# Performance work log

Measured on AMD Instinct MI355X. Metric: run time of the kernel, lower is better.

Reference implementation:

```python
import jax, jax.numpy as jnp
import numpy as np
from jax import lax

K_NN = 16      # neighbors used by compute_knn_distance
ANCHOR_K = 64  # config['anchor_k']


def _knn_dist_vec(pts):
    """compute_knn_distance for one object: mean offset vector to K_NN nearest neighbors.
    pts: (N, 3) -> (N, 3)"""
    sq = jnp.sum(pts * pts, axis=-1)                      # (N,)
    d2 = sq[:, None] + sq[None, :] - 2.0 * (pts @ pts.T)  # (N, N) squared dists
    n = pts.shape[0]
    d2 = d2 + jnp.eye(n, dtype=pts.dtype) * 1e10          # exclude self
    _, idx = lax.top_k(-d2, K_NN)                          # (N, K_NN) nearest indices
    neigh = pts[idx]                                       # (N, K_NN, 3)
    return jnp.mean(neigh - pts[:, None, :], axis=1)       # (N, 3)


def _fps(pts, k):
    """Farthest point sampling for one object. pts: (N, 3) -> (k,) int32 indices."""
    d0 = jnp.sum((pts - pts[0]) ** 2, axis=-1)             # dist to seed point 0

    def step(min_d, _):
        idx = jnp.argmax(min_d)
        d = jnp.sum((pts - pts[idx]) ** 2, axis=-1)
        return jnp.minimum(min_d, d), idx

    _, idxs = lax.scan(step, d0, None, length=k - 1)
    return jnp.concatenate([jnp.zeros((1,), dtype=idxs.dtype), idxs])


def setup_inputs() -> dict:
    key = jax.random.key(0)
    k1, k2, k3, k4 = jax.random.split(key, 4)
    B, N_obj, N_v = 4, 8, 2048
    positions = jax.random.normal(k1, (B, N_obj, N_v, 3), dtype=jnp.float32)
    velocities = jax.random.normal(k2, (B, N_obj, N_v, 3), dtype=jnp.float32)
    physics_params = jax.random.uniform(k3, (B, N_obj, 3), dtype=jnp.float32)
    # reference pose at t=0: nearby but distinct so rel_pos is nontrivial
    ref_positions = positions + 0.05 * jax.random.normal(k4, (B, N_obj, N_v, 3), dtype=jnp.float32)
    return {"positions": positions, "velocities": velocities,
            "physics_params": physics_params, "ref_positions": ref_positions}


def reference(positions, velocities, physics_params, ref_positions):
    B, N_obj, N_v, _ = positions.shape
    flat = positions.reshape(B * N_obj, N_v, 3)

    # pairwise KNN distance feature per point
    dist_vec = jax.vmap(_knn_dist_vec)(flat).reshape(B, N_obj, N_v, 3)

    # iterative FPS anchor sampling (vectorized over all B*N_obj objects)
    anchors = jax.vmap(lambda p: _fps(p, ANCHOR_K))(flat).reshape(B, N_obj, ANCHOR_K)

    rel_pos = positions - ref_positions

    # multi-field gather at anchor indices (torch.gather on dim=2)
    gather = lambda f: jnp.take_along_axis(f, anchors[..., None], axis=2)
    anchor_dist = gather(dist_vec)       # (B, N_obj, K, 3)
    anchor_vel = gather(velocities)      # (B, N_obj, K, 3)
    anchor_rel = gather(rel_pos)         # (B, N_obj, K, 3)

    phys = jnp.broadcast_to(physics_params[:, :, None, :], (B, N_obj, ANCHOR_K, 3))
    query = jnp.concatenate([anchor_dist, anchor_vel, anchor_rel, phys], axis=-1)  # (B, N_obj, K, 12)
    return query
```

## Files before the change

### kernel.cpp

```cpp
#include <hip/hip_runtime.h>
#include <stdint.h>

#define NPTS 2048
#define KNN  16
#define AK   64
#define TPB  256
#define FPT  (NPTS / TPB)
#define KPL  (NPTS / 64)

typedef unsigned long long u64;
typedef unsigned int u32;

__device__ __forceinline__ float sq3(float x, float y, float z) {
    return __fadd_rn(__fadd_rn(__fmul_rn(x, x), __fmul_rn(y, y)), __fmul_rn(z, z));
}

__global__ __launch_bounds__(TPB) void fps_kernel(const float* __restrict__ pos,
                                                  int* __restrict__ anchors) {
    const int obj = blockIdx.x;
    const int t = threadIdx.x;
    __shared__ float sp[NPTS * 3];
    __shared__ u64 skey[8];

    {
        const float4* g4 = (const float4*)(pos + (size_t)obj * NPTS * 3);
        float4* s4 = (float4*)sp;
        #pragma unroll
        for (int i = 0; i < 6; i++) s4[t + i * TPB] = g4[t + i * TPB];
    }
    __syncthreads();

    float px[FPT], py[FPT], pz[FPT], mind[FPT];
    {
        const float ax0 = sp[0], ay0 = sp[1], az0 = sp[2];
        #pragma unroll
        for (int i = 0; i < FPT; i++) {
            const int j = t + i * TPB;
            px[i] = sp[j * 3 + 0];
            py[i] = sp[j * 3 + 1];
            pz[i] = sp[j * 3 + 2];
            mind[i] = sq3(__fsub_rn(px[i], ax0), __fsub_rn(py[i], ay0),
                          __fsub_rn(pz[i], az0));
        }
    }
    if (t == 0) anchors[obj * AK + 0] = 0;

    for (int s = 1; s < AK; s++) {
        float bv = mind[0];
        u32 slot = 0;
        #pragma unroll
        for (int i = 1; i < FPT; i++)
            if (mind[i] > bv) { bv = mind[i]; slot = (u32)i; }
        const u32 j = (u32)t + slot * TPB;
        u64 key = ((u64)__float_as_uint(bv) << 32) | (u32)(~j);

        #pragma unroll
        for (int off = 32; off > 0; off >>= 1) {
            const u64 o = (u64)__shfl_xor((long long)key, off, 64);
            if (o > key) key = o;
        }

        u64* sk = &skey[(s & 1) * 4];
        if ((t & 63) == 0) sk[t >> 6] = key;
        __syncthreads();

        u64 k = sk[0];
        if (sk[1] > k) k = sk[1];
        if (sk[2] > k) k = sk[2];
        if (sk[3] > k) k = sk[3];
        const int idx = (int)(~(u32)k);
        if (t == 0) anchors[obj * AK + s] = idx;

        const float bx = sp[idx * 3 + 0];
        const float by = sp[idx * 3 + 1];
        const float bz = sp[idx * 3 + 2];
        #pragma unroll
        for (int i = 0; i < FPT; i++) {
            const float d2 = sq3(__fsub_rn(px[i], bx), __fsub_rn(py[i], by),
                                 __fsub_rn(pz[i], bz));
            mind[i] = fminf(mind[i], d2);
        }
    }
}

__global__ __launch_bounds__(TPB) void knn_gather_kernel(
    const float* __restrict__ pos, const float* __restrict__ vel,
    const float* __restrict__ phys, const float* __restrict__ refp,
    const int* __restrict__ anchors, float* __restrict__ out) {
    const int t = threadIdx.x;
    const int wid = t >> 6, lane = t & 63;
    const int g = blockIdx.x * 4 + wid;
    const int obj = g >> 6;

    __shared__ float sp[NPTS * 3];
    {
        const float4* g4 = (const float4*)(pos + (size_t)obj * NPTS * 3);
        float4* s4 = (float4*)sp;
        #pragma unroll
        for (int i = 0; i < 6; i++) s4[t + i * TPB] = g4[t + i * TPB];
    }
    const int a = anchors[g];
    __syncthreads();

    const float ax = sp[a * 3 + 0], ay = sp[a * 3 + 1], az = sp[a * 3 + 2];
    const float sqa = sq3(ax, ay, az);

    u32 b[KPL];
    #pragma unroll
    for (int i = 0; i < KPL; i++) {
        const int j = lane + i * 64;
        const float x = sp[j * 3 + 0], y = sp[j * 3 + 1], z = sp[j * 3 + 2];
        const float sqj = sq3(x, y, z);
        const float dot = __fadd_rn(
            __fadd_rn(__fmul_rn(ax, x), __fmul_rn(ay, y)), __fmul_rn(az, z));
        const float d2 = __fsub_rn(__fadd_rn(sqa, sqj), __fmul_rn(2.0f, dot));
        u32 bb = __float_as_uint(d2);
        bb ^= (bb & 0x80000000u) ? 0xFFFFFFFFu : 0x80000000u;
        b[i] = (j == a) ? 0xFFFFFFFFu : bb;
    }

    float sx = 0.0f, sy = 0.0f, sz = 0.0f;
    int winj = -1;

    for (int r = 0; r < KNN; r++) {
        const int wm = winj - lane;
        u32 bv = 0xFFFFFFFFu;
        u32 slot = 0;
        #pragma unroll
        for (int i = 0; i < KPL; i++) {
            if (wm == i * 64) b[i] = 0xFFFFFFFFu;
            if (b[i] < bv) { bv = b[i]; slot = (u32)i; }
        }
        u64 key = ((u64)bv << 32) | (u32)(lane + slot * 64);
        #pragma unroll
        for (int off = 32; off > 0; off >>= 1) {
            const u64 o = (u64)__shfl_xor((long long)key, off, 64);
            if (o < key) key = o;
        }
        winj = (int)(u32)key;

        const float wx = sp[winj * 3 + 0];
        const float wy = sp[winj * 3 + 1];
        const float wz = sp[winj * 3 + 2];
        sx = __fadd_rn(sx, __fsub_rn(wx, ax));
        sy = __fadd_rn(sy, __fsub_rn(wy, ay));
        sz = __fadd_rn(sz, __fsub_rn(wz, az));
    }

    if (lane == 0) {
        float* o = out + (size_t)g * 12;
        o[0] = __fmul_rn(sx, 0.0625f);
        o[1] = __fmul_rn(sy, 0.0625f);
        o[2] = __fmul_rn(sz, 0.0625f);
        const size_t base = (size_t)obj * NPTS * 3 + (size_t)a * 3;
        o[3] = vel[base + 0];
        o[4] = vel[base + 1];
        o[5] = vel[base + 2];
        o[6] = __fsub_rn(pos[base + 0], refp[base + 0]);
        o[7] = __fsub_rn(pos[base + 1], refp[base + 1]);
        o[8] = __fsub_rn(pos[base + 2], refp[base + 2]);
        const float* ph = phys + (size_t)obj * 3;
        o[9]  = ph[0];
        o[10] = ph[1];
        o[11] = ph[2];
    }
}

extern "C" void kernel_launch(void* const* d_in, const int* in_sizes, int n_in,
                              void* d_out, int out_size, void* d_ws, size_t ws_size,
                              hipStream_t stream) {
    const float* pos  = (const float*)d_in[0];
    const float* vel  = (const float*)d_in[1];
    const float* phys = (const float*)d_in[2];
    const float* refp = (const float*)d_in[3];
    float* out = (float*)d_out;

    const int n_obj = in_sizes[2] / 3;
    int* anchors = (int*)d_ws;

    fps_kernel<<<n_obj, TPB, 0, stream>>>(pos, anchors);
    knn_gather_kernel<<<n_obj * AK / 4, TPB, 0, stream>>>(pos, vel, phys, refp,
                                                          anchors, out);
}
```

Measured before the change: 115.5 us.

## Use DPP wave reductions, SoA shared layout, fused FPS argmax, per-lane top-4 KNN cache

FPS now folds the argmax into the distance-update loop. It also publishes each wave winner's coordinates alongside its key, so the post-barrier LDS lookup goes away. Both kernels store points in structure-of-arrays shared memory and use DPP-based wave reductions in place of some shuffles. In KNN, each lane keeps a sorted cache of its four smallest keys, so most rounds need only a wave min with no rescan of all 32 candidates; a lane rescans only when its cache runs dry. The catch is 64-bit keys that raise register pressure, and uncoalesced strided global loads into SoA.

Result: faster. 109.6 us (-5.2%).

```diff
diff --git a/kernel.cpp b/kernel.cpp
--- a/kernel.cpp
+++ b/kernel.cpp
@@ -10,76 +10,112 @@
 
 typedef unsigned long long u64;
 typedef unsigned int u32;
+#define UMAX 0xFFFFFFFFFFFFFFFFull
 
 __device__ __forceinline__ float sq3(float x, float y, float z) {
     return __fadd_rn(__fadd_rn(__fmul_rn(x, x), __fmul_rn(y, y)), __fmul_rn(z, z));
+}
+
+template <int CTRL>
+__device__ __forceinline__ u64 dpp64(u64 k) {
+    const int lo = __builtin_amdgcn_update_dpp((int)(u32)k, (int)(u32)k,
+                                               CTRL, 0xF, 0xF, false);
+    const int hi = __builtin_amdgcn_update_dpp((int)(u32)(k >> 32),
+                                               (int)(u32)(k >> 32),
+                                               CTRL, 0xF, 0xF, false);
+    return ((u64)(u32)hi << 32) | (u32)lo;
+}
+
+__device__ __forceinline__ u64 wave_max64(u64 k) {
+    u64 o;
+    o = dpp64<0xB1>(k);  if (o > k) k = o;
+    o = dpp64<0x4E>(k);  if (o > k) k = o;
+    o = dpp64<0x141>(k); if (o > k) k = o;
+    o = dpp64<0x140>(k); if (o > k) k = o;
+    o = (u64)__shfl_xor((long long)k, 16, 64); if (o > k) k = o;
+    o = (u64)__shfl_xor((long long)k, 32, 64); if (o > k) k = o;
+    return k;
+}
+
+__device__ __forceinline__ u64 wave_min64(u64 k) {
+    u64 o;
+    o = dpp64<0xB1>(k);  if (o < k) k = o;
+    o = dpp64<0x4E>(k);  if (o < k) k = o;
+    o = dpp64<0x141>(k); if (o < k) k = o;
+    o = dpp64<0x140>(k); if (o < k) k = o;
+    o = (u64)__shfl_xor((long long)k, 16, 64); if (o < k) k = o;
+    o = (u64)__shfl_xor((long long)k, 32, 64); if (o < k) k = o;
+    return k;
 }
 
 __global__ __launch_bounds__(TPB) void fps_kernel(const float* __restrict__ pos,
                                                   int* __restrict__ anchors) {
     const int obj = blockIdx.x;
     const int t = threadIdx.x;
-    __shared__ float sp[NPTS * 3];
+    const int wid = t >> 6, lane = t & 63;
+
+    __shared__ float sX[NPTS], sY[NPTS], sZ[NPTS];
     __shared__ u64 skey[8];
-
+    __shared__ float4 scrd[8];
+
+    const float* pts = pos + (size_t)obj * NPTS * 3;
+    #pragma unroll
+    for (int i = 0; i < FPT; i++) {
+        const int j = t + i * TPB;
+        sX[j] = pts[j * 3 + 0];
+        sY[j] = pts[j * 3 + 1];
+        sZ[j] = pts[j * 3 + 2];
+    }
+    __syncthreads();
+
+    float px[FPT], py[FPT], pz[FPT], mind[FPT];
+    u64 key;
     {
-        const float4* g4 = (const float4*)(pos + (size_t)obj * NPTS * 3);
-        float4* s4 = (float4*)sp;
-        #pragma unroll
-        for (int i = 0; i < 6; i++) s4[t + i * TPB] = g4[t + i * TPB];
-    }
-    __syncthreads();
-
-    float px[FPT], py[FPT], pz[FPT], mind[FPT];
-    {
-        const float ax0 = sp[0], ay0 = sp[1], az0 = sp[2];
+        const float ax0 = sX[0], ay0 = sY[0], az0 = sZ[0];
+        float bv = -1.0f; u32 bj = 0;
         #pragma unroll
         for (int i = 0; i < FPT; i++) {
             const int j = t + i * TPB;
-            px[i] = sp[j * 3 + 0];
-            py[i] = sp[j * 3 + 1];
-            pz[i] = sp[j * 3 + 2];
-            mind[i] = sq3(__fsub_rn(px[i], ax0), __fsub_rn(py[i], ay0),
-                          __fsub_rn(pz[i], az0));
-        }
+            px[i] = sX[j]; py[i] = sY[j]; pz[i] = sZ[j];
+            const float d2 = sq3(__fsub_rn(px[i], ax0), __fsub_rn(py[i], ay0),
+                                 __fsub_rn(pz[i], az0));
+            mind[i] = d2;
+            if (d2 > bv) { bv = d2; bj = (u32)j; }
+        }
+        key = ((u64)__float_as_uint(bv) << 32) | (u32)(~bj);
     }
     if (t == 0) anchors[obj * AK + 0] = 0;
 
     for (int s = 1; s < AK; s++) {
-        float bv = mind[0];
-        u32 slot = 0;
-        #pragma unroll
-        for (int i = 1; i < FPT; i++)
-            if (mind[i] > bv) { bv = mind[i]; slot = (u32)i; }
-        const u32 j = (u32)t + slot * TPB;
-        u64 key = ((u64)__float_as_uint(bv) << 32) | (u32)(~j);
-
-        #pragma unroll
-        for (int off = 32; off > 0; off >>= 1) {
-            const u64 o = (u64)__shfl_xor((long long)key, off, 64);
-            if (o > key) key = o;
-        }
-
-        u64* sk = &skey[(s & 1) * 4];
-        if ((t & 63) == 0) sk[t >> 6] = key;
+        const u64 wk = wave_max64(key);
+        const int side = (s & 1) * 4;
+        if (lane == 0) {
+            const int widx = (int)(~(u32)wk);
+            skey[side + wid] = wk;
+            scrd[side + wid] = make_float4(sX[widx], sY[widx], sZ[widx], 0.f);
+        }
         __syncthreads();
-
-        u64 k = sk[0];
-        if (sk[1] > k) k = sk[1];
-        if (sk[2] > k) k = sk[2];
-        if (sk[3] > k) k = sk[3];
-        const int idx = (int)(~(u32)k);
-        if (t == 0) anchors[obj * AK + s] = idx;
-
-        const float bx = sp[idx * 3 + 0];
-        const float by = sp[idx * 3 + 1];
-        const float bz = sp[idx * 3 + 2];
+        u64 ka = skey[side + 0];
+        float4 ca = scrd[side + 0];
+        { const u64 k1 = skey[side + 1]; const float4 q = scrd[side + 1];
+          if (k1 > ka) { ka = k1; ca = q; } }
+        { const u64 k2 = skey[side + 2]; const float4 q = scrd[side + 2];
+          if (k2 > ka) { ka = k2; ca = q; } }
+        { const u64 k3 = skey[side + 3]; const float4 q = scrd[side + 3];
+          if (k3 > ka) { ka = k3; ca = q; } }
+        if (t == 0) anchors[obj * AK + s] = (int)(~(u32)ka);
+        if (s == AK - 1) break;
+
+        float bv = -1.0f; u32 bj = 0;
         #pragma unroll
         for (int i = 0; i < FPT; i++) {
-            const float d2 = sq3(__fsub_rn(px[i], bx), __fsub_rn(py[i], by),
-                                 __fsub_rn(pz[i], bz));
-            mind[i] = fminf(mind[i], d2);
-        }
+            const float d2 = sq3(__fsub_rn(px[i], ca.x), __fsub_rn(py[i], ca.y),
+                                 __fsub_rn(pz[i], ca.z));
+            const float nm = fminf(mind[i], d2);
+            mind[i] = nm;
+            if (nm > bv) { bv = nm; bj = (u32)(t + i * TPB); }
+        }
+        key = ((u64)__float_as_uint(bv) << 32) | (u32)(~bj);
     }
 }
 
@@ -92,66 +128,88 @@
     const int g = blockIdx.x * 4 + wid;
     const int obj = g >> 6;
 
-    __shared__ float sp[NPTS * 3];
-    {
-        const float4* g4 = (const float4*)(pos + (size_t)obj * NPTS * 3);
-        float4* s4 = (float4*)sp;
-        #pragma unroll
-        for (int i = 0; i < 6; i++) s4[t + i * TPB] = g4[t + i * TPB];
+    __shared__ float sX[NPTS], sY[NPTS], sZ[NPTS];
+    const float* pts = pos + (size_t)obj * NPTS * 3;
+    #pragma unroll
+    for (int i = 0; i < FPT; i++) {
+        const int j = t + i * TPB;
+        sX[j] = pts[j * 3 + 0];
+        sY[j] = pts[j * 3 + 1];
+        sZ[j] = pts[j * 3 + 2];
     }
     const int a = anchors[g];
     __syncthreads();
 
-    const float ax = sp[a * 3 + 0], ay = sp[a * 3 + 1], az = sp[a * 3 + 2];
+    const float ax = sX[a], ay = sY[a], az = sZ[a];
     const float sqa = sq3(ax, ay, az);
 
-    u32 b[KPL];
+    u64 k[KPL];
     #pragma unroll
     for (int i = 0; i < KPL; i++) {
         const int j = lane + i * 64;
-        const float x = sp[j * 3 + 0], y = sp[j * 3 + 1], z = sp[j * 3 + 2];
+        const float x = sX[j], y = sY[j], z = sZ[j];
         const float sqj = sq3(x, y, z);
         const float dot = __fadd_rn(
             __fadd_rn(__fmul_rn(ax, x), __fmul_rn(ay, y)), __fmul_rn(az, z));
         const float d2 = __fsub_rn(__fadd_rn(sqa, sqj), __fmul_rn(2.0f, dot));
         u32 bb = __float_as_uint(d2);
         bb ^= (bb & 0x80000000u) ? 0xFFFFFFFFu : 0x80000000u;
-        b[i] = (j == a) ? 0xFFFFFFFFu : bb;
-    }
-
-    float sx = 0.0f, sy = 0.0f, sz = 0.0f;
-    int winj = -1;
-
+        k[i] = (j == a) ? UMAX : (((u64)bb << 32) | (u32)j);
+    }
+
+    u64 c0 = UMAX, c1 = UMAX, c2 = UMAX, c3 = UMAX;
+    #pragma unroll
+    for (int i = 0; i < KPL; i++) c0 = (k[i] < c0) ? k[i] : c0;
+    #pragma unroll
+    for (int i = 0; i < KPL; i++) {
+        const u64 v = (k[i] > c0) ? k[i] : UMAX; c1 = (v < c1) ? v : c1;
+    }
+    #pragma unroll
+    for (int i = 0; i < KPL; i++) {
+        const u64 v = (k[i] > c1) ? k[i] : UMAX; c2 = (v < c2) ? v : c2;
+    }
+    #pragma unroll
+    for (int i = 0; i < KPL; i++) {
+        const u64 v = (k[i] > c2) ? k[i] : UMAX; c3 = (v < c3) ? v : c3;
+    }
+
+    float accx = 0.f, accy = 0.f, accz = 0.f;
+    u64 thr = 0;
     for (int r = 0; r < KNN; r++) {
-        const int wm = winj - lane;
-        u32 bv = 0xFFFFFFFFu;
-        u32 slot = 0;
-        #pragma unroll
-        for (int i = 0; i < KPL; i++) {
-            if (wm == i * 64) b[i] = 0xFFFFFFFFu;
-            if (b[i] < bv) { bv = b[i]; slot = (u32)i; }
-        }
-        u64 key = ((u64)bv << 32) | (u32)(lane + slot * 64);
-        #pragma unroll
-        for (int off = 32; off > 0; off >>= 1) {
-            const u64 o = (u64)__shfl_xor((long long)key, off, 64);
-            if (o < key) key = o;
-        }
-        winj = (int)(u32)key;
-
-        const float wx = sp[winj * 3 + 0];
-        const float wy = sp[winj * 3 + 1];
-        const float wz = sp[winj * 3 + 2];
-        sx = __fadd_rn(sx, __fsub_rn(wx, ax));
-        sy = __fadd_rn(sy, __fsub_rn(wy, ay));
-        sz = __fadd_rn(sz, __fsub_rn(wz, az));
+        if (c0 == UMAX) {
+            #pragma unroll
+            for (int i = 0; i < KPL; i++) {
+                const u64 v = (k[i] > thr) ? k[i] : UMAX; c0 = (v < c0) ? v : c0;
+            }
+            #pragma unroll
+            for (int i = 0; i < KPL; i++) {
+                const u64 v = (k[i] > c0) ? k[i] : UMAX; c1 = (v < c1) ? v : c1;
+            }
+            #pragma unroll
+            for (int i = 0; i < KPL; i++) {
+                const u64 v = (k[i] > c1) ? k[i] : UMAX; c2 = (v < c2) ? v : c2;
+            }
+            #pragma unroll
+            for (int i = 0; i < KPL; i++) {
+                const u64 v = (k[i] > c2) ? k[i] : UMAX; c3 = (v < c3) ? v : c3;
+            }
+        }
+        const u64 w = wave_min64(c0);
+        const int winj = (int)(u32)w;
+        const float wx = sX[winj], wy = sY[winj], wz = sZ[winj];
+        accx = __fadd_rn(accx, __fsub_rn(wx, ax));
+        accy = __fadd_rn(accy, __fsub_rn(wy, ay));
+        accz = __fadd_rn(accz, __fsub_rn(wz, az));
+        if (c0 == w) {
+            thr = c0; c0 = c1; c1 = c2; c2 = c3; c3 = UMAX;
+        }
     }
 
     if (lane == 0) {
         float* o = out + (size_t)g * 12;
-        o[0] = __fmul_rn(sx, 0.0625f);
-        o[1] = __fmul_rn(sy, 0.0625f);
-        o[2] = __fmul_rn(sz, 0.0625f);
+        o[0] = __fmul_rn(accx, 0.0625f);
+        o[1] = __fmul_rn(accy, 0.0625f);
+        o[2] = __fmul_rn(accz, 0.0625f);
         const size_t base = (size_t)obj * NPTS * 3 + (size_t)a * 3;
         o[3] = vel[base + 0];
         o[4] = vel[base + 1];
```
